# Kernel optimization log

Hardware: AMD Instinct MI355X
Metric: run time of the kernel (lower is better)

Reference implementation:

```python
import jax, jax.numpy as jnp
import numpy as np

N = 100000   # num 'note' nodes
E = 1000000  # edges per relation
R = 3        # relation types (onset, consecutive, during)
IN = 128
OUT = 64
NEG_SLOPE = 0.2  # GATConv default leaky_relu slope


def setup_inputs() -> dict:
    key = jax.random.key(0)
    ks = jax.random.split(key, 13)
    x = jax.random.normal(ks[0], (N, IN), jnp.float32)
    ei0 = jax.random.randint(ks[1], (2, E), 0, N)
    ei1 = jax.random.randint(ks[2], (2, E), 0, N)
    ei2 = jax.random.randint(ks[3], (2, E), 0, N)
    s1 = 1.0 / np.sqrt(IN)
    s2 = 1.0 / np.sqrt(OUT)
    W1 = jax.random.normal(ks[4], (R, IN, OUT), jnp.float32) * s1
    a_src1 = jax.random.normal(ks[5], (R, OUT), jnp.float32) * s2
    a_dst1 = jax.random.normal(ks[6], (R, OUT), jnp.float32) * s2
    b1 = jnp.zeros((R, OUT), jnp.float32)
    W2 = jax.random.normal(ks[7], (R, OUT, OUT), jnp.float32) * s2
    a_src2 = jax.random.normal(ks[8], (R, OUT), jnp.float32) * s2
    a_dst2 = jax.random.normal(ks[9], (R, OUT), jnp.float32) * s2
    b2 = jnp.zeros((R, OUT), jnp.float32)
    return dict(x=x, ei0=ei0, ei1=ei1, ei2=ei2,
                W1=W1, a_src1=a_src1, a_dst1=a_dst1, b1=b1,
                W2=W2, a_src2=a_src2, a_dst2=a_dst2, b2=b2)


def _gat_relation(x, ei, W, a_src, a_dst, b):
    # single-head GATConv for one relation (aggr='sum' over edges)
    h = x @ W                              # [N, OUT]
    src, dst = ei[0], ei[1]
    al_src = h @ a_src                     # [N]
    al_dst = h @ a_dst                     # [N]
    e = jax.nn.leaky_relu(al_src[src] + al_dst[dst], NEG_SLOPE)  # [E]
    # segment softmax over incoming edges per destination node
    m = jax.ops.segment_max(e, dst, num_segments=N)              # [N]
    num = jnp.exp(e - m[dst])                                    # [E]
    den = jax.ops.segment_sum(num, dst, num_segments=N)          # [N]
    coef = num / den[dst]                                        # [E]
    msg = coef[:, None] * h[src]                                 # [E, OUT]
    return jax.ops.segment_sum(msg, dst, num_segments=N) + b     # [N, OUT]


def _hetero_layer(x, eis, W, a_src, a_dst, b):
    # to_hetero: per-relation GATConv, then mean across relations
    outs = [_gat_relation(x, eis[r], W[r], a_src[r], a_dst[r], b[r]) for r in range(R)]
    return jnp.mean(jnp.stack(outs, 0), 0)


def _l2norm(v):
    # F.normalize(v, dim=-1), eps=1e-12
    n = jnp.linalg.norm(v, axis=-1, keepdims=True)
    return v / jnp.maximum(n, 1e-12)


def reference(x, ei0, ei1, ei2, W1, a_src1, a_dst1, b1, W2, a_src2, a_dst2, b2):
    eis = [ei0, ei1, ei2]
    h = _hetero_layer(x, eis, W1, a_src1, a_dst1, b1)
    h = jax.nn.relu(_l2norm(h))  # dropout is identity in eval mode
    out = _hetero_layer(h, eis, W2, a_src2, a_dst2, b2)
    return out  # x_dict['note']
```

## Files before the change

kernel.cpp:

```cpp
#include <hip/hip_runtime.h>
#include <hip/hip_bf16.h>
#include <hip/hip_fp16.h>
#include <math.h>

constexpr int NN = 100000;
constexpr int EE = 1000000;
constexpr int RRR = 3;
constexpr int DIN = 128;
constexpr int DOUT = 64;
constexpr float SLOPE = 0.2f;
constexpr int NR = RRR * NN;
constexpr int BSEG = 256;
constexpr int NBUCK = (NR + BSEG - 1) / BSEG;
constexpr int BCAP = 4096;
constexpr int CHUNK_E = 8192;
constexpr int NCH_PER_R = (EE + CHUNK_E - 1) / CHUNK_E;
constexpr int NCH = RRR * NCH_PER_R;
constexpr int MT = NBUCK * NCH;
constexpr int SCAN_CHUNK = 1024;
constexpr int NSCB = (MT + SCAN_CHUNK - 1) / SCAN_CHUNK;

using f16x8 = __attribute__((ext_vector_type(8))) _Float16;
using f32x4 = __attribute__((ext_vector_type(4))) float;

template<int CTRL>
__device__ __forceinline__ float dppf(float v) {
    return __int_as_float(__builtin_amdgcn_update_dpp(
        __float_as_int(v), __float_as_int(v), CTRL, 0xf, 0xf, false));
}
__device__ __forceinline__ float dpp_allred_add16(float v) {
    v += dppf<0xB1>(v);
    v += dppf<0x4E>(v);
    v += dppf<0x141>(v);
    v += dppf<0x140>(v);
    return v;
}
__device__ __forceinline__ float dpp_allred_max16(float v) {
    v = fmaxf(v, dppf<0xB1>(v));
    v = fmaxf(v, dppf<0x4E>(v));
    v = fmaxf(v, dppf<0x141>(v));
    v = fmaxf(v, dppf<0x140>(v));
    return v;
}

__global__ __launch_bounds__(256) void pack_W(
    const float* __restrict__ W1, const float* __restrict__ W2,
    __half* __restrict__ Wp1, __half* __restrict__ Wp2)
{
    int r = blockIdx.x;
    for (int i = threadIdx.x; i < 4 * 4 * 512; i += 256) {
        int j = i & 7, lane = (i >> 3) & 63, nt = (i >> 9) & 3, ks = i >> 11;
        int k = ks * 32 + (lane >> 4) * 8 + j, c = nt * 16 + (lane & 15);
        Wp1[((size_t)r * 16 + ks * 4 + nt) * 512 + lane * 8 + j] = __float2half(W1[(r * DIN + k) * 64 + c]);
    }
    for (int i = threadIdx.x; i < 2 * 4 * 512; i += 256) {
        int j = i & 7, lane = (i >> 3) & 63, nt = (i >> 9) & 3, ks = i >> 11;
        int k = ks * 32 + (lane >> 4) * 8 + j, c = nt * 16 + (lane & 15);
        Wp2[((size_t)r * 8 + ks * 4 + nt) * 512 + lane * 8 + j] = __float2half(W2[(r * DOUT + k) * 64 + c]);
    }
}

template<int K, typename AT>
__global__ __launch_bounds__(256) void gemm_mfma2(
    const AT* __restrict__ xin,
    const __half* __restrict__ Wp,
    const float* __restrict__ asrc, const float* __restrict__ adst,
    __half* __restrict__ h,
    float* __restrict__ als, float* __restrict__ ald)
{
    constexpr int KS = K / 32;
    __shared__ float outb[64 * 65];
    const int t = threadIdx.x;
    const int lane = t & 63;
    const int w = t >> 6;
    const int row0 = blockIdx.x * 64;

    const int kgrp = lane >> 4;
    const int l15 = lane & 15;
    int arow = row0 + w * 16 + l15; if (arow >= NN) arow = NN - 1;

    f16x8 a[KS];
    if constexpr (sizeof(AT) == 2) {
        const __half* ab = (const __half*)xin + (size_t)arow * K + kgrp * 8;
#pragma unroll
        for (int ks = 0; ks < KS; ++ks) a[ks] = *(const f16x8*)(ab + ks * 32);
    } else {
        const float* ab = (const float*)xin + (size_t)arow * K + kgrp * 8;
#pragma unroll
        for (int ks = 0; ks < KS; ++ks) {
            float4 lo = *(const float4*)(ab + ks * 32);
            float4 hi = *(const float4*)(ab + ks * 32 + 4);
            union { f16x8 v; __half2 p[4]; } u;
            u.p[0] = __floats2half2_rn(lo.x, lo.y);
            u.p[1] = __floats2half2_rn(lo.z, lo.w);
            u.p[2] = __floats2half2_rn(hi.x, hi.y);
            u.p[3] = __floats2half2_rn(hi.z, hi.w);
            a[ks] = u.v;
        }
    }

    const int nrows = (NN - row0 < 64) ? (NN - row0) : 64;

#pragma unroll
    for (int r = 0; r < RRR; ++r) {
        const __half* wbase = Wp + ((size_t)r * KS * 4) * 512 + lane * 8;
        f32x4 acc[4] = {};
#pragma unroll
        for (int ks = 0; ks < KS; ++ks) {
#pragma unroll
            for (int nt = 0; nt < 4; ++nt) {
                f16x8 b = *(const f16x8*)(wbase + (size_t)(ks * 4 + nt) * 512);
                acc[nt] = __builtin_amdgcn_mfma_f32_16x16x32_f16(a[ks], b, acc[nt], 0, 0, 0);
            }
        }

        {
            float ps[4] = {0.f, 0.f, 0.f, 0.f}, pd[4] = {0.f, 0.f, 0.f, 0.f};
#pragma unroll
            for (int nt = 0; nt < 4; ++nt) {
                int c = l15 + 16 * nt;
                float a_ = asrc[r * 64 + c], d_ = adst[r * 64 + c];
#pragma unroll
                for (int i = 0; i < 4; ++i) {
                    ps[i] = fmaf(acc[nt][i], a_, ps[i]);
                    pd[i] = fmaf(acc[nt][i], d_, pd[i]);
                }
            }
#pragma unroll
            for (int o = 8; o; o >>= 1) {
#pragma unroll
                for (int i = 0; i < 4; ++i) {
                    ps[i] += __shfl_xor(ps[i], o);
                    pd[i] += __shfl_xor(pd[i], o);
                }
            }
            if (l15 == 0) {
#pragma unroll
                for (int i = 0; i < 4; ++i) {
                    int row = row0 + w * 16 + kgrp * 4 + i;
                    if (row < NN) { als[r * NN + row] = ps[i]; ald[r * NN + row] = pd[i]; }
                }
            }
        }

#pragma unroll
        for (int nt = 0; nt < 4; ++nt)
#pragma unroll
            for (int i = 0; i < 4; ++i)
                outb[(w * 16 + kgrp * 4 + i) * 65 + l15 + 16 * nt] = acc[nt][i];
        __syncthreads();

        __half2* h2 = (__half2*)(h + ((size_t)r * NN + row0) * 64);
        for (int idx = t; idx < nrows * 32; idx += 256) {
            int row = idx >> 5, cc = idx & 31;
            h2[row * 32 + cc] = __floats2half2_rn(outb[row * 65 + cc * 2], outb[row * 65 + cc * 2 + 1]);
        }
        __syncthreads();
    }
}


__global__ __launch_bounds__(256) void chunk_hist(
    const int* __restrict__ ei0, const int* __restrict__ ei1, const int* __restrict__ ei2,
    unsigned* __restrict__ M)
{
    __shared__ unsigned hist[NBUCK];
    const int r = blockIdx.y, bx = blockIdx.x;
    const int* ei = (r == 0) ? ei0 : ((r == 1) ? ei1 : ei2);
    const int t = threadIdx.x;
    for (int i = t; i < NBUCK; i += 256) hist[i] = 0;
    __syncthreads();
    const int e0 = bx * CHUNK_E;
    const int e1 = (e0 + CHUNK_E < EE) ? e0 + CHUNK_E : EE;
    for (int e = e0 + t; e < e1; e += 256) {
        int idx = r * NN + ei[EE + e];
        atomicAdd(&hist[idx >> 8], 1u);
    }
    __syncthreads();
    const int c = r * NCH_PER_R + bx;
    for (int i = t; i < NBUCK; i += 256) M[(size_t)i * NCH + c] = hist[i];
}

__global__ __launch_bounds__(256) void scan_block(unsigned* __restrict__ data, unsigned* __restrict__ bsum)
{
    __shared__ unsigned tsum[256];
    const int base = blockIdx.x * SCAN_CHUNK;
    const int t = threadIdx.x;
    const int i0 = base + t * 4;
    unsigned v[4];
#pragma unroll
    for (int k = 0; k < 4; ++k) v[k] = (i0 + k < MT) ? data[i0 + k] : 0u;
    unsigned run = 0;
#pragma unroll
    for (int k = 0; k < 4; ++k) { unsigned x = v[k]; v[k] = run; run += x; }
    tsum[t] = run;
    __syncthreads();
    unsigned val = run;
    for (int d = 1; d < 256; d <<= 1) {
        unsigned add = (t >= d) ? tsum[t - d] : 0u;
        __syncthreads();
        val += add;
        tsum[t] = val;
        __syncthreads();
    }
    unsigned texcl = val - run;
    if (t == 255) bsum[blockIdx.x] = val;
#pragma unroll
    for (int k = 0; k < 4; ++k)
        if (i0 + k < MT) data[i0 + k] = texcl + v[k];
}

__global__ __launch_bounds__(256) void scan_bsums(unsigned* __restrict__ bsum)
{
    __shared__ unsigned s[NSCB];
    int t = threadIdx.x;
    for (int i = t; i < NSCB; i += 256) s[i] = bsum[i];
    __syncthreads();
    if (t == 0) {
        unsigned run = 0;
        for (int i = 0; i < NSCB; ++i) { unsigned x = s[i]; s[i] = run; run += x; }
    }
    __syncthreads();
    for (int i = t; i < NSCB; i += 256) bsum[i] = s[i];
}

__global__ __launch_bounds__(256) void add_off(unsigned* __restrict__ data, const unsigned* __restrict__ bsum)
{
    int i = blockIdx.x * 256 + threadIdx.x;
    if (i >= MT) return;
    data[i] += bsum[i / SCAN_CHUNK];
}

__global__ __launch_bounds__(256) void chunk_scatter(
    const int* __restrict__ ei0, const int* __restrict__ ei1, const int* __restrict__ ei2,
    const unsigned* __restrict__ Ms, unsigned* __restrict__ packed)
{
    __shared__ unsigned cur[NBUCK];
    const int r = blockIdx.y, bx = blockIdx.x;
    const int* ei = (r == 0) ? ei0 : ((r == 1) ? ei1 : ei2);
    const int t = threadIdx.x;
    const int c = r * NCH_PER_R + bx;
    for (int i = t; i < NBUCK; i += 256) cur[i] = Ms[(size_t)i * NCH + c];
    __syncthreads();
    const int e0 = bx * CHUNK_E;
    const int e1 = (e0 + CHUNK_E < EE) ? e0 + CHUNK_E : EE;
    for (int e = e0 + t; e < e1; e += 256) {
        int src = ei[e];
        int idx = r * NN + ei[EE + e];
        unsigned pos = atomicAdd(&cur[idx >> 8], 1u);
        packed[pos] = (unsigned)src | ((unsigned)(idx & 255) << 24);
    }
}

__global__ __launch_bounds__(256) void bucket_build(
    unsigned* __restrict__ packed,
    const unsigned* __restrict__ Ms,
    unsigned* __restrict__ off)
{
    __shared__ unsigned sp[BCAP];
    __shared__ unsigned ssrc[BCAP];
    __shared__ unsigned scnt[BSEG];
    __shared__ unsigned scur[BSEG];
    __shared__ unsigned tsum[BSEG];
    const int b = blockIdx.x;
    const int t = threadIdx.x;
    const unsigned base = Ms[(size_t)b * NCH];
    const unsigned next = (b + 1 < NBUCK) ? Ms[(size_t)(b + 1) * NCH] : (unsigned)((size_t)RRR * EE);
    int cnt = (int)(next - base);
    if (cnt > BCAP) cnt = BCAP;
    for (int i = t; i < cnt; i += 256) sp[i] = packed[base + i];
    scnt[t] = 0;
    __syncthreads();
    for (int i = t; i < cnt; i += 256) atomicAdd(&scnt[sp[i] >> 24], 1u);
    __syncthreads();
    unsigned v = scnt[t];
    tsum[t] = v;
    __syncthreads();
    unsigned val = v;
    for (int d = 1; d < 256; d <<= 1) {
        unsigned add = (t >= d) ? tsum[t - d] : 0u;
        __syncthreads();
        val += add;
        tsum[t] = val;
        __syncthreads();
    }
    unsigned excl = val - v;
    scur[t] = excl;
    const int segs = (NR - b * BSEG < BSEG) ? (NR - b * BSEG) : BSEG;
    if (t < segs) off[b * BSEG + t] = base + excl;
    __syncthreads();
    for (int i = t; i < cnt; i += 256) {
        unsigned p = sp[i];
        unsigned pos = atomicAdd(&scur[p >> 24], 1u);
        ssrc[pos] = p & 0x00FFFFFFu;
    }
    __syncthreads();
    for (int i = t; i < cnt; i += 256) packed[base + i] = ssrc[i];
}

template<bool L1>
__global__ __launch_bounds__(256) void aggregate8(
    const int* __restrict__ csr_src, const unsigned* __restrict__ off,
    const __half* __restrict__ h,
    const float* __restrict__ als, const float* __restrict__ ald,
    const float* __restrict__ bias,
    float* __restrict__ outp,
    __half* __restrict__ outH)
{
    __shared__ float sbuf[4][64];
    const int wid = threadIdx.x >> 6;
    const int node = blockIdx.x * 4 + wid;
    if (node >= NN) return;
    const int lane = threadIdx.x & 63;
    const int sub = lane >> 4;
    const int fc = lane & 15;

    unsigned start[RRR]; int cnt[RRR]; float aldv[RRR];
    int maxcnt = 0;
#pragma unroll
    for (int r = 0; r < RRR; ++r) {
        int idx = r * NN + node;
        unsigned s = off[idx];
        unsigned e = (idx == NR - 1) ? (unsigned)((size_t)RRR * EE) : off[idx + 1];
        start[r] = s; cnt[r] = (int)(e - s); aldv[r] = ald[idx];
        if (cnt[r] > maxcnt) maxcnt = cnt[r];
    }

    float4 total = make_float4(0.f, 0.f, 0.f, 0.f);

    if (maxcnt <= 64) {
        int srcv[RRR]; float lr[RRR];
#pragma unroll
        for (int r = 0; r < RRR; ++r) {
            bool act = lane < cnt[r];
            int s_ = act ? csr_src[start[r] + lane] : 0;
            srcv[r] = s_;
            float sv = act ? (als[r * NN + s_] + aldv[r]) : -3.0e38f;
            lr[r] = (sv > 0.f) ? sv : SLOPE * sv;
        }
        float m[RRR];
#pragma unroll
        for (int r = 0; r < RRR; ++r) m[r] = dpp_allred_max16(lr[r]);
#pragma unroll
        for (int r = 0; r < RRR; ++r) m[r] = fmaxf(m[r], __shfl_xor(m[r], 16));
#pragma unroll
        for (int r = 0; r < RRR; ++r) m[r] = fmaxf(m[r], __shfl_xor(m[r], 32));

        float p[RRR], den[RRR];
#pragma unroll
        for (int r = 0; r < RRR; ++r) {
            p[r] = (lane < cnt[r]) ? __expf(lr[r] - m[r]) : 0.f;
            den[r] = dpp_allred_add16(p[r]);
        }
#pragma unroll
        for (int r = 0; r < RRR; ++r) den[r] += __shfl_xor(den[r], 16);
#pragma unroll
        for (int r = 0; r < RRR; ++r) den[r] += __shfl_xor(den[r], 32);

        float4 tp = make_float4(0.f, 0.f, 0.f, 0.f);
#pragma unroll
        for (int r = 0; r < RRR; ++r) {
            float inv = (cnt[r] > 0) ? 1.f / den[r] : 0.f;
            const __half* hr = h + (size_t)r * NN * DOUT;
            float4 acc = make_float4(0.f, 0.f, 0.f, 0.f);
            const int nq = (cnt[r] + 15) >> 4;
            for (int q = 0; q < nq; ++q) {
                const int base = q * 16;
                float pl[4]; int sl[4];
#pragma unroll
                for (int l = 0; l < 4; ++l) {
                    int e = base + l * 4 + sub;
                    pl[l] = __shfl(p[r], e);
                    sl[l] = __shfl(srcv[r], e);
                }
                uint2 rl[4];
#pragma unroll
                for (int l = 0; l < 4; ++l)
                    rl[l] = *(const uint2*)(hr + (size_t)sl[l] * DOUT + fc * 4);
#pragma unroll
                for (int l = 0; l < 4; ++l) {
                    float2 f01 = __half22float2(*(const __half2*)&rl[l].x);
                    float2 f23 = __half22float2(*(const __half2*)&rl[l].y);
                    acc.x = fmaf(pl[l], f01.x, acc.x);
                    acc.y = fmaf(pl[l], f01.y, acc.y);
                    acc.z = fmaf(pl[l], f23.x, acc.z);
                    acc.w = fmaf(pl[l], f23.y, acc.w);
                }
            }
            tp.x = fmaf(inv, acc.x, tp.x);
            tp.y = fmaf(inv, acc.y, tp.y);
            tp.z = fmaf(inv, acc.z, tp.z);
            tp.w = fmaf(inv, acc.w, tp.w);
        }
        tp.x += __shfl_xor(tp.x, 16); tp.y += __shfl_xor(tp.y, 16);
        tp.z += __shfl_xor(tp.z, 16); tp.w += __shfl_xor(tp.w, 16);
        tp.x += __shfl_xor(tp.x, 32); tp.y += __shfl_xor(tp.y, 32);
        tp.z += __shfl_xor(tp.z, 32); tp.w += __shfl_xor(tp.w, 32);
        total = tp;
    } else {
        float totalS = 0.f;
#pragma unroll
        for (int r = 0; r < RRR; ++r) {
            if (cnt[r] <= 0) continue;
            const __half* hr = h + (size_t)r * NN * DOUT;
            const float* alsr = als + (size_t)r * NN;
            float m = -3.4e38f, den = 0.f, accv = 0.f;
            for (int t0 = 0; t0 < cnt[r]; t0 += 64) {
                int j = t0 + lane;
                bool act = (j < cnt[r]);
                int src = 0;
                float lrv = -3.4e38f;
                if (act) {
                    src = csr_src[start[r] + j];
                    float sv = alsr[src] + aldv[r];
                    lrv = (sv > 0.f) ? sv : SLOPE * sv;
                }
                float mt = lrv;
#pragma unroll
                for (int o = 32; o; o >>= 1) mt = fmaxf(mt, __shfl_xor(mt, o));
                float mnew = fmaxf(m, mt);
                float scale = __expf(m - mnew);
                den *= scale; accv *= scale; m = mnew;
                float p = act ? __expf(lrv - m) : 0.f;
                float ps = p;
#pragma unroll
                for (int o = 32; o; o >>= 1) ps += __shfl_xor(ps, o);
                den += ps;
                int tcnt = cnt[r] - t0; if (tcnt > 64) tcnt = 64;
                for (int j2 = 0; j2 < tcnt; ++j2) {
                    int sj = __builtin_amdgcn_readlane(src, j2);
                    float pj = __int_as_float(__builtin_amdgcn_readlane(__float_as_int(p), j2));
                    accv = fmaf(pj, __half2float(hr[(size_t)sj * DOUT + lane]), accv);
                }
            }
            totalS += accv / den;
        }
        sbuf[wid][lane] = totalS;
        __builtin_amdgcn_s_waitcnt(0);
        total = *(const float4*)&sbuf[wid][fc * 4];
    }

    float4 b4 = make_float4(0.f, 0.f, 0.f, 0.f);
#pragma unroll
    for (int r = 0; r < RRR; ++r) {
        float4 bb = *(const float4*)(bias + r * DOUT + fc * 4);
        b4.x += bb.x; b4.y += bb.y; b4.z += bb.z; b4.w += bb.w;
    }
    float4 v;
    v.x = (total.x + b4.x) * (1.f / 3.f);
    v.y = (total.y + b4.y) * (1.f / 3.f);
    v.z = (total.z + b4.z) * (1.f / 3.f);
    v.w = (total.w + b4.w) * (1.f / 3.f);
    if (L1) {
        float ss = v.x * v.x + v.y * v.y + v.z * v.z + v.w * v.w;
        ss = dpp_allred_add16(ss);
        float di = 1.f / fmaxf(sqrtf(ss), 1e-12f);
        v.x = fmaxf(v.x * di, 0.f);
        v.y = fmaxf(v.y * di, 0.f);
        v.z = fmaxf(v.z * di, 0.f);
        v.w = fmaxf(v.w * di, 0.f);
        if (sub == 0) {
            __half2* o2 = (__half2*)(outH + (size_t)node * DOUT + fc * 4);
            o2[0] = __floats2half2_rn(v.x, v.y);
            o2[1] = __floats2half2_rn(v.z, v.w);
        }
    } else {
        if (sub == 0) *(float4*)(outp + (size_t)node * DOUT + fc * 4) = v;
    }
}

extern "C" void kernel_launch(void* const* d_in, const int* in_sizes, int n_in,
                              void* d_out, int out_size, void* d_ws, size_t ws_size,
                              hipStream_t stream) {
    const float* x   = (const float*)d_in[0];
    const int* ei0   = (const int*)d_in[1];
    const int* ei1   = (const int*)d_in[2];
    const int* ei2   = (const int*)d_in[3];
    const float* W1  = (const float*)d_in[4];
    const float* as1 = (const float*)d_in[5];
    const float* ad1 = (const float*)d_in[6];
    const float* b1  = (const float*)d_in[7];
    const float* W2  = (const float*)d_in[8];
    const float* as2 = (const float*)d_in[9];
    const float* ad2 = (const float*)d_in[10];
    const float* b2  = (const float*)d_in[11];
    float* out = (float*)d_out;

    float* ws = (float*)d_ws;
    size_t off_u = 0;
    __half* h       = (__half*)(ws + off_u); off_u += (size_t)RRR * NN * DOUT / 2;
    float* als      = ws + off_u; off_u += (size_t)RRR * NN;
    float* ald      = ws + off_u; off_u += (size_t)RRR * NN;
    unsigned* packed= (unsigned*)(ws + off_u); off_u += (size_t)RRR * EE;
    unsigned* off   = (unsigned*)(ws + off_u); off_u += NR;
    __half* hmid_h  = (__half*)(ws + off_u); off_u += (size_t)NN * DOUT / 2;
    __half* Wp1     = (__half*)(ws + off_u); off_u += (3 * 16 * 512) / 2;
    __half* Wp2     = (__half*)(ws + off_u); off_u += (3 * 8 * 512) / 2;
    unsigned* M     = (unsigned*)(ws + off_u); off_u += MT;
    unsigned* bsum  = (unsigned*)(ws + off_u); off_u += NSCB + 8;

    dim3 blk(256);
    int gG = (NN + 63) / 64;
    dim3 gC(NCH_PER_R, RRR);
    int gA = NN / 4;

    chunk_hist<<<gC, blk, 0, stream>>>(ei0, ei1, ei2, M);
    scan_block<<<NSCB, blk, 0, stream>>>(M, bsum);
    scan_bsums<<<1, blk, 0, stream>>>(bsum);
    add_off<<<(MT + 255) / 256, blk, 0, stream>>>(M, bsum);
    chunk_scatter<<<gC, blk, 0, stream>>>(ei0, ei1, ei2, M, packed);
    bucket_build<<<NBUCK, blk, 0, stream>>>(packed, M, off);
    const int* csr_src = (const int*)packed;

    pack_W<<<3, blk, 0, stream>>>(W1, W2, Wp1, Wp2);

    gemm_mfma2<DIN, float><<<gG, blk, 0, stream>>>(x, Wp1, as1, ad1, h, als, ald);
    aggregate8<true><<<gA, blk, 0, stream>>>(csr_src, off, h, als, ald, b1, out, hmid_h);

    gemm_mfma2<DOUT, __half><<<gG, blk, 0, stream>>>(hmid_h, Wp2, as2, ad2, h, als, ald);
    aggregate8<false><<<gA, blk, 0, stream>>>(csr_src, off, h, als, ald, b2, out, hmid_h);
}
```

Measured before the change: 301.6 us.

## Process two destination nodes per wavefront in GAT aggregation kernel

The aggregation kernel now maps two destination nodes to each 64-lane wavefront, one per 32-lane half, instead of one node per wavefront. The fast path handles up to 32 in-edges per relation and needs only intra-half reductions. If any lane exceeds that, the whole wave falls back to a serial per-node online-softmax loop over both nodes. With about 10 edges per node on average, this aims to cut idle lanes and double node throughput per wave. The cost is that a single high-degree node forces both nodes onto the slow path.

```diff
diff --git a/kernel.cpp b/kernel.cpp
--- a/kernel.cpp
+++ b/kernel.cpp
@@ -299,7 +299,7 @@
 }
 
 template<bool L1>
-__global__ __launch_bounds__(256) void aggregate8(
+__global__ __launch_bounds__(256) void aggregate9(
     const int* __restrict__ csr_src, const unsigned* __restrict__ off,
     const __half* __restrict__ h,
     const float* __restrict__ als, const float* __restrict__ ald,
@@ -309,11 +309,12 @@
 {
     __shared__ float sbuf[4][64];
     const int wid = threadIdx.x >> 6;
-    const int node = blockIdx.x * 4 + wid;
-    if (node >= NN) return;
     const int lane = threadIdx.x & 63;
-    const int sub = lane >> 4;
-    const int fc = lane & 15;
+    const int nh = lane >> 5;
+    const int l31 = lane & 31;
+    const int sub = l31 >> 4;
+    const int fc = l31 & 15;
+    const int node = blockIdx.x * 8 + wid * 2 + nh;
 
     unsigned start[RRR]; int cnt[RRR]; float aldv[RRR];
     int maxcnt = 0;
@@ -328,12 +329,12 @@
 
     float4 total = make_float4(0.f, 0.f, 0.f, 0.f);
 
-    if (maxcnt <= 64) {
+    if (__all(maxcnt <= 32)) {
         int srcv[RRR]; float lr[RRR];
 #pragma unroll
         for (int r = 0; r < RRR; ++r) {
-            bool act = lane < cnt[r];
-            int s_ = act ? csr_src[start[r] + lane] : 0;
+            bool act = l31 < cnt[r];
+            int s_ = act ? csr_src[start[r] + l31] : 0;
             srcv[r] = s_;
             float sv = act ? (als[r * NN + s_] + aldv[r]) : -3.0e38f;
             lr[r] = (sv > 0.f) ? sv : SLOPE * sv;
@@ -343,19 +344,15 @@
         for (int r = 0; r < RRR; ++r) m[r] = dpp_allred_max16(lr[r]);
 #pragma unroll
         for (int r = 0; r < RRR; ++r) m[r] = fmaxf(m[r], __shfl_xor(m[r], 16));
-#pragma unroll
-        for (int r = 0; r < RRR; ++r) m[r] = fmaxf(m[r], __shfl_xor(m[r], 32));
 
         float p[RRR], den[RRR];
 #pragma unroll
         for (int r = 0; r < RRR; ++r) {
-            p[r] = (lane < cnt[r]) ? __expf(lr[r] - m[r]) : 0.f;
+            p[r] = (l31 < cnt[r]) ? __expf(lr[r] - m[r]) : 0.f;
             den[r] = dpp_allred_add16(p[r]);
         }
 #pragma unroll
         for (int r = 0; r < RRR; ++r) den[r] += __shfl_xor(den[r], 16);
-#pragma unroll
-        for (int r = 0; r < RRR; ++r) den[r] += __shfl_xor(den[r], 32);
 
         float4 tp = make_float4(0.f, 0.f, 0.f, 0.f);
 #pragma unroll
@@ -363,15 +360,15 @@
             float inv = (cnt[r] > 0) ? 1.f / den[r] : 0.f;
             const __half* hr = h + (size_t)r * NN * DOUT;
             float4 acc = make_float4(0.f, 0.f, 0.f, 0.f);
-            const int nq = (cnt[r] + 15) >> 4;
+            const int nq = (cnt[r] + 7) >> 3;
             for (int q = 0; q < nq; ++q) {
-                const int base = q * 16;
+                const int base = q * 8;
                 float pl[4]; int sl[4];
 #pragma unroll
                 for (int l = 0; l < 4; ++l) {
-                    int e = base + l * 4 + sub;
-                    pl[l] = __shfl(p[r], e);
-                    sl[l] = __shfl(srcv[r], e);
+                    int e = base + l * 2 + sub;
+                    pl[l] = __shfl(p[r], nh * 32 + e);
+                    sl[l] = __shfl(srcv[r], nh * 32 + e);
                 }
                 uint2 rl[4];
 #pragma unroll
@@ -394,50 +391,57 @@
         }
         tp.x += __shfl_xor(tp.x, 16); tp.y += __shfl_xor(tp.y, 16);
         tp.z += __shfl_xor(tp.z, 16); tp.w += __shfl_xor(tp.w, 16);
-        tp.x += __shfl_xor(tp.x, 32); tp.y += __shfl_xor(tp.y, 32);
-        tp.z += __shfl_xor(tp.z, 32); tp.w += __shfl_xor(tp.w, 32);
         total = tp;
     } else {
-        float totalS = 0.f;
-#pragma unroll
-        for (int r = 0; r < RRR; ++r) {
-            if (cnt[r] <= 0) continue;
-            const __half* hr = h + (size_t)r * NN * DOUT;
-            const float* alsr = als + (size_t)r * NN;
-            float m = -3.4e38f, den = 0.f, accv = 0.f;
-            for (int t0 = 0; t0 < cnt[r]; t0 += 64) {
-                int j = t0 + lane;
-                bool act = (j < cnt[r]);
-                int src = 0;
-                float lrv = -3.4e38f;
-                if (act) {
-                    src = csr_src[start[r] + j];
-                    float sv = alsr[src] + aldv[r];
-                    lrv = (sv > 0.f) ? sv : SLOPE * sv;
+        for (int nn = 0; nn < 2; ++nn) {
+            int node2 = blockIdx.x * 8 + wid * 2 + nn;
+            float totalS = 0.f;
+#pragma unroll
+            for (int r = 0; r < RRR; ++r) {
+                int idx = r * NN + node2;
+                unsigned s2 = off[idx];
+                unsigned e2 = (idx == NR - 1) ? (unsigned)((size_t)RRR * EE) : off[idx + 1];
+                int c2 = (int)(e2 - s2);
+                if (c2 <= 0) continue;
+                float aldv2 = ald[idx];
+                const __half* hr = h + (size_t)r * NN * DOUT;
+                const float* alsr = als + (size_t)r * NN;
+                float m = -3.4e38f, den = 0.f, accv = 0.f;
+                for (int t0 = 0; t0 < c2; t0 += 64) {
+                    int j = t0 + lane;
+                    bool act = (j < c2);
+                    int src = 0;
+                    float lrv = -3.4e38f;
+                    if (act) {
+                        src = csr_src[s2 + j];
+                        float sv = alsr[src] + aldv2;
+                        lrv = (sv > 0.f) ? sv : SLOPE * sv;
+                    }
+                    float mt = lrv;
+#pragma unroll
+                    for (int o = 32; o; o >>= 1) mt = fmaxf(mt, __shfl_xor(mt, o));
+                    float mnew = fmaxf(m, mt);
+                    float scale = __expf(m - mnew);
+                    den *= scale; accv *= scale; m = mnew;
+                    float pp = act ? __expf(lrv - m) : 0.f;
+                    float ps = pp;
+#pragma unroll
+                    for (int o = 32; o; o >>= 1) ps += __shfl_xor(ps, o);
+                    den += ps;
+                    int tcnt = c2 - t0; if (tcnt > 64) tcnt = 64;
+                    for (int j2 = 0; j2 < tcnt; ++j2) {
+                        int sj = __builtin_amdgcn_readlane(src, j2);
+                        float pj = __int_as_float(__builtin_amdgcn_readlane(__float_as_int(pp), j2));
+                        accv = fmaf(pj, __half2float(hr[(size_t)sj * DOUT + lane]), accv);
+                    }
                 }
-                float mt = lrv;
-#pragma unroll
-                for (int o = 32; o; o >>= 1) mt = fmaxf(mt, __shfl_xor(mt, o));
-                float mnew = fmaxf(m, mt);
-                float scale = __expf(m - mnew);
-                den *= scale; accv *= scale; m = mnew;
-                float p = act ? __expf(lrv - m) : 0.f;
-                float ps = p;
-#pragma unroll
-                for (int o = 32; o; o >>= 1) ps += __shfl_xor(ps, o);
-                den += ps;
-                int tcnt = cnt[r] - t0; if (tcnt > 64) tcnt = 64;
-                for (int j2 = 0; j2 < tcnt; ++j2) {
-                    int sj = __builtin_amdgcn_readlane(src, j2);
-                    float pj = __int_as_float(__builtin_amdgcn_readlane(__float_as_int(p), j2));
-                    accv = fmaf(pj, __half2float(hr[(size_t)sj * DOUT + lane]), accv);
-                }
+                totalS += accv / den;
             }
-            totalS += accv / den;
-        }
-        sbuf[wid][lane] = totalS;
-        __builtin_amdgcn_s_waitcnt(0);
-        total = *(const float4*)&sbuf[wid][fc * 4];
+            sbuf[wid][lane] = totalS;
+            __builtin_amdgcn_s_waitcnt(0);
+            if (nh == nn) total = *(const float4*)&sbuf[wid][fc * 4];
+            __builtin_amdgcn_s_waitcnt(0);
+        }
     }
 
     float4 b4 = make_float4(0.f, 0.f, 0.f, 0.f);
@@ -502,7 +506,7 @@
     dim3 blk(256);
     int gG = (NN + 63) / 64;
     dim3 gC(NCH_PER_R, RRR);
-    int gA = NN / 4;
+    int gA = (NN + 7) / 8;
 
     chunk_hist<<<gC, blk, 0, stream>>>(ei0, ei1, ei2, M);
     scan_block<<<NSCB, blk, 0, stream>>>(M, bsum);
@@ -515,8 +519,8 @@
     pack_W<<<3, blk, 0, stream>>>(W1, W2, Wp1, Wp2);
 
     gemm_mfma2<DIN, float><<<gG, blk, 0, stream>>>(x, Wp1, as1, ad1, h, als, ald);
-    aggregate8<true><<<gA, blk, 0, stream>>>(csr_src, off, h, als, ald, b1, out, hmid_h);
+    aggregate9<true><<<gA, blk, 0, stream>>>(csr_src, off, h, als, ald, b1, out, hmid_h);
 
     gemm_mfma2<DOUT, __half><<<gG, blk, 0, stream>>>(hmid_h, Wp2, as2, ad2, h, als, ald);
-    aggregate8<false><<<gA, blk, 0, stream>>>(csr_src, off, h, als, ald, b2, out, hmid_h);
-}
+    aggregate9<false><<<gA, blk, 0, stream>>>(csr_src, off, h, als, ald, b2, out, hmid_h);
+}
```

New measurement: 266.2 us. 1.13x faster.
